# Performance work log

Hardware: AMD Instinct MI355X
Metric: run time of the kernel (lower is better)

The kernel has to match this reference:

```python
import jax, jax.numpy as jnp
import numpy as np

N, E, OBS, H, MSG, A = 20000, 640000, 64, 256, 128, 16


def setup_inputs() -> dict:
    key = jax.random.key(0)
    ks = jax.random.split(key, 16)
    s = lambda fan_in: 1.0 / np.sqrt(fan_in)
    inp = {
        'feat': jax.random.normal(ks[0], (N, OBS), jnp.float32),
        'h': jax.random.normal(ks[1], (N, H), jnp.float32),
        'src': jax.random.randint(ks[2], (E,), 0, N, jnp.int32),
        'dst': jax.random.randint(ks[3], (E,), 0, N, jnp.int32),
        # DenseObservationEncoder: 2 Linear+ReLU layers
        'enc_W0': jax.random.uniform(ks[4], (OBS, H), jnp.float32, -s(OBS), s(OBS)),
        'enc_b0': jnp.zeros((H,), jnp.float32),
        'enc_W1': jax.random.uniform(ks[5], (H, H), jnp.float32, -s(H), s(H)),
        'enc_b1': jnp.zeros((H,), jnp.float32),
        # BaseComm.f_msg: Linear(2H -> MSG)
        'msg_W': jax.random.uniform(ks[6], (2 * H, MSG), jnp.float32, -s(2 * H), s(2 * H)),
        'msg_b': jnp.zeros((MSG,), jnp.float32),
        # BaseComm.f_udt: GRUCell(H+MSG -> H), torch gate order r,z,n
        'gru_Wih': jax.random.uniform(ks[7], (H + MSG, 3 * H), jnp.float32, -s(H), s(H)),
        'gru_Whh': jax.random.uniform(ks[8], (H, 3 * H), jnp.float32, -s(H), s(H)),
        'gru_bih': jnp.zeros((3 * H,), jnp.float32),
        'gru_bhh': jnp.zeros((3 * H,), jnp.float32),
        # f_out: Linear(H -> n_actions)
        'out_W': jax.random.uniform(ks[9], (H, A), jnp.float32, -s(H), s(H)),
        'out_b': jnp.zeros((A,), jnp.float32),
    }
    return inp


def _gru_cell(u, h, Wih, Whh, bih, bhh):
    gi = u @ Wih + bih          # [N, 3H]
    gh = h @ Whh + bhh          # [N, 3H]
    i_r, i_z, i_n = jnp.split(gi, 3, axis=1)
    h_r, h_z, h_n = jnp.split(gh, 3, axis=1)
    r = jax.nn.sigmoid(i_r + h_r)
    z = jax.nn.sigmoid(i_z + h_z)
    n = jnp.tanh(i_n + r * h_n)
    return (1.0 - z) * n + z * h


def reference(feat, h, src, dst, enc_W0, enc_b0, enc_W1, enc_b1,
              msg_W, msg_b, gru_Wih, gru_Whh, gru_bih, gru_bhh,
              out_W, out_b):
    n_nodes = feat.shape[0]
    # encoder MLP
    x = jax.nn.relu(feat @ enc_W0 + enc_b0)
    x = jax.nn.relu(x @ enc_W1 + enc_b1)            # [N, H]
    h_det = jax.lax.stop_gradient(h)
    # edge messages: f_msg(cat(x[src], h_det[src])) done as split matmul to avoid the concat copy
    Wx, Wh = msg_W[:x.shape[1]], msg_W[x.shape[1]:]
    msg = x[src] @ Wx + h_det[src] @ Wh + msg_b     # [E, MSG]
    # mean aggregation into destination mailboxes (zero for isolated nodes, like DGL)
    sums = jax.ops.segment_sum(msg, dst, num_segments=n_nodes)          # [N, MSG]
    cnt = jax.ops.segment_sum(jnp.ones_like(dst, jnp.float32), dst, num_segments=n_nodes)
    c = sums / jnp.maximum(cnt, 1.0)[:, None]
    # GRU update
    u = jnp.concatenate([x, c], axis=1)             # [N, H+MSG]
    h_new = _gru_cell(u, h, gru_Wih, gru_Whh, gru_bih, gru_bhh)
    q = h_new @ out_W + out_b                       # [N, n_actions]
    return q, h_new
```

## Files before the change

### kernel.cpp

```cpp
#include <hip/hip_runtime.h>

#define N_NODES 20000
#define N_EDGES 640000
#define OBS 64
#define HDIM 256
#define MSGD 128
#define ADIM 16
#define Q_OFF 0
#define HN_OFF (N_NODES * ADIM)
#define DEG_PAD 128
#define CNT_STRIDE 16

typedef __bf16 bf16x8 __attribute__((ext_vector_type(8)));
typedef float  f32x4  __attribute__((ext_vector_type(4)));

__device__ __forceinline__ unsigned short f2bf(float f) {
    union { float f; unsigned int i; } v; v.f = f;
    unsigned int i = v.i;
    return (unsigned short)((i + 0x7fffu + ((i >> 16) & 1u)) >> 16);
}
__device__ __forceinline__ float bf2f(unsigned short u) {
    union { unsigned int i; float f; } v; v.i = ((unsigned int)u) << 16; return v.f;
}
__device__ __forceinline__ bf16x8 ld8(const unsigned short* p) {
    bf16x8 r;
    __builtin_memcpy(&r, __builtin_assume_aligned(p, 16), 16);
    return r;
}
__device__ __forceinline__ f32x4 mfma16(bf16x8 a, bf16x8 b, f32x4 c) {
    return __builtin_amdgcn_mfma_f32_16x16x32_bf16(a, b, c, 0, 0, 0);
}
__device__ __forceinline__ float sigmoidf_(float x) { return 1.0f / (1.0f + __expf(-x)); }
__device__ __forceinline__ float tanhf_(float x) { return 2.0f / (1.0f + __expf(-2.0f * x)) - 1.0f; }

__device__ __forceinline__ int packIdx(int row, int k, int Kc) {
    return ((row >> 4) * Kc + (k >> 5)) * 512 + (((k >> 3) & 3) * 16 + (row & 15)) * 8 + (k & 7);
}
__device__ __forceinline__ int packIdxEp(int tile, int rlow, int t, int lr, int Kc) {
    return (tile * Kc + (t >> 1)) * 512 + (((t & 1) * 2 + (lr >> 3)) * 16 + rlow) * 8 + (lr & 7);
}
__device__ __forceinline__ int packIdxLoc(int rlow, int t, int lr) {
    return (t >> 1) * 512 + (((t & 1) * 2 + (lr >> 3)) * 16 + rlow) * 8 + (lr & 7);
}

#define WS_W0P    0u
#define WS_W1P    32768u
#define WS_WMP    163840u
#define WS_WGP    294912u
#define WS_WOP    1277952u
#define WS_FEATP  1286144u
#define WS_HBP    3846144u
#define WS_XP     24326144u
#define WS_MN     34566144u
#define WS_CP     39686144u
#define WS_HNP    44806144u
#define WS_CNT    55046144u

#define GATE_STRIDE 163840

__global__ __launch_bounds__(256) void setup_kernel(
    const float* __restrict__ feat, const float* __restrict__ h,
    const float* __restrict__ w0, const float* __restrict__ w1, const float* __restrict__ wm,
    const float* __restrict__ wih, const float* __restrict__ whh, const float* __restrict__ wo,
    unsigned short* __restrict__ featp, unsigned short* __restrict__ hbp,
    unsigned short* __restrict__ w0p, unsigned short* __restrict__ w1p,
    unsigned short* __restrict__ wmp, unsigned short* __restrict__ wgp,
    unsigned short* __restrict__ wop)
{
    const int tid = blockIdx.x * 256 + threadIdx.x;
    const int np = gridDim.x * 256;

    for (int it = tid; it < 5000 * 8; it += np) {
        int rowq = it >> 3, kb = it & 7;
        int row0 = rowq * 4, k = kb * 8;
        uint4 vv[4];
        #pragma unroll
        for (int j = 0; j < 4; ++j) {
            const float4* p = (const float4*)(feat + (row0 + j) * OBS + k);
            float4 a = p[0], b = p[1];
            union { unsigned short u[8]; uint4 v; } r;
            r.u[0]=f2bf(a.x); r.u[1]=f2bf(a.y); r.u[2]=f2bf(a.z); r.u[3]=f2bf(a.w);
            r.u[4]=f2bf(b.x); r.u[5]=f2bf(b.y); r.u[6]=f2bf(b.z); r.u[7]=f2bf(b.w);
            vv[j] = r.v;
        }
        uint4* dp = (uint4*)(featp + packIdx(row0, k, 2));
        dp[0]=vv[0]; dp[1]=vv[1]; dp[2]=vv[2]; dp[3]=vv[3];
    }
    for (int it = tid; it < 5000 * 32; it += np) {
        int rowq = it >> 5, kb = it & 31;
        int row0 = rowq * 4, k = kb * 8;
        uint4 vv[4];
        #pragma unroll
        for (int j = 0; j < 4; ++j) {
            const float4* p = (const float4*)(h + (row0 + j) * HDIM + k);
            float4 a = p[0], b = p[1];
            union { unsigned short u[8]; uint4 v; } r;
            r.u[0]=f2bf(a.x); r.u[1]=f2bf(a.y); r.u[2]=f2bf(a.z); r.u[3]=f2bf(a.w);
            r.u[4]=f2bf(b.x); r.u[5]=f2bf(b.y); r.u[6]=f2bf(b.z); r.u[7]=f2bf(b.w);
            vv[j] = r.v;
        }
        uint4* dp = (uint4*)(hbp + packIdx(row0, k, 8));
        dp[0]=vv[0]; dp[1]=vv[1]; dp[2]=vv[2]; dp[3]=vv[3];
    }
    for (int it = tid; it < 512; it += np) {
        int nq = it & 63, kb = it >> 6;
        unsigned short u[4][8];
        #pragma unroll
        for (int j = 0; j < 8; ++j) {
            float4 f = *(const float4*)(w0 + (kb * 8 + j) * 256 + nq * 4);
            u[0][j]=f2bf(f.x); u[1][j]=f2bf(f.y); u[2][j]=f2bf(f.z); u[3][j]=f2bf(f.w);
        }
        uint4* dp = (uint4*)(w0p + packIdx(nq * 4, kb * 8, 2));
        #pragma unroll
        for (int n = 0; n < 4; ++n) { uint4 v; __builtin_memcpy(&v, u[n], 16); dp[n] = v; }
    }
    for (int it = tid; it < 2048; it += np) {
        int nq = it & 63, kb = it >> 6;
        unsigned short u[4][8];
        #pragma unroll
        for (int j = 0; j < 8; ++j) {
            float4 f = *(const float4*)(w1 + (kb * 8 + j) * 256 + nq * 4);
            u[0][j]=f2bf(f.x); u[1][j]=f2bf(f.y); u[2][j]=f2bf(f.z); u[3][j]=f2bf(f.w);
        }
        uint4* dp = (uint4*)(w1p + packIdx(nq * 4, kb * 8, 8));
        #pragma unroll
        for (int n = 0; n < 4; ++n) { uint4 v; __builtin_memcpy(&v, u[n], 16); dp[n] = v; }
    }
    for (int it = tid; it < 2048; it += np) {
        int nq = it & 31, kb = it >> 5;
        unsigned short u[4][8];
        #pragma unroll
        for (int j = 0; j < 8; ++j) {
            float4 f = *(const float4*)(wm + (kb * 8 + j) * 128 + nq * 4);
            u[0][j]=f2bf(f.x); u[1][j]=f2bf(f.y); u[2][j]=f2bf(f.z); u[3][j]=f2bf(f.w);
        }
        uint4* dp = (uint4*)(wmp + packIdx(nq * 4, kb * 8, 16));
        #pragma unroll
        for (int n = 0; n < 4; ++n) { uint4 v; __builtin_memcpy(&v, u[n], 16); dp[n] = v; }
    }
    for (int it = tid; it < 9216; it += np) {
        int c3q = it % 192, kb = it / 192;
        int n4 = c3q * 4, gate = n4 >> 8, nn = n4 & 255;
        unsigned short u[4][8];
        #pragma unroll
        for (int j = 0; j < 8; ++j) {
            float4 f = *(const float4*)(wih + (kb * 8 + j) * 768 + n4);
            u[0][j]=f2bf(f.x); u[1][j]=f2bf(f.y); u[2][j]=f2bf(f.z); u[3][j]=f2bf(f.w);
        }
        uint4* dp = (uint4*)(wgp + gate * GATE_STRIDE + packIdx(nn, kb * 8, 20));
        #pragma unroll
        for (int n = 0; n < 4; ++n) { uint4 v; __builtin_memcpy(&v, u[n], 16); dp[n] = v; }
    }
    for (int it = tid; it < 6144; it += np) {
        int c3q = it % 192, kb = it / 192;
        int n4 = c3q * 4, gate = n4 >> 8, nn = n4 & 255;
        unsigned short u[4][8];
        #pragma unroll
        for (int j = 0; j < 8; ++j) {
            float4 f = *(const float4*)(whh + (kb * 8 + j) * 768 + n4);
            u[0][j]=f2bf(f.x); u[1][j]=f2bf(f.y); u[2][j]=f2bf(f.z); u[3][j]=f2bf(f.w);
        }
        uint4* dp = (uint4*)(wgp + gate * GATE_STRIDE + packIdx(nn, 384 + kb * 8, 20));
        #pragma unroll
        for (int n = 0; n < 4; ++n) { uint4 v; __builtin_memcpy(&v, u[n], 16); dp[n] = v; }
    }
    for (int it = tid; it < 128; it += np) {
        int nq = it & 3, kb = it >> 2;
        unsigned short u[4][8];
        #pragma unroll
        for (int j = 0; j < 8; ++j) {
            float4 f = *(const float4*)(wo + (kb * 8 + j) * 16 + nq * 4);
            u[0][j]=f2bf(f.x); u[1][j]=f2bf(f.y); u[2][j]=f2bf(f.z); u[3][j]=f2bf(f.w);
        }
        uint4* dp = (uint4*)(wop + packIdx(nq * 4, kb * 8, 8));
        #pragma unroll
        for (int n = 0; n < 4; ++n) { uint4 v; __builtin_memcpy(&v, u[n], 16); dp[n] = v; }
    }
}

__global__ __launch_bounds__(256) void enc_scatter_kernel(
    const unsigned short* __restrict__ featp, const unsigned short* __restrict__ hbp,
    const unsigned short* __restrict__ w0p, const float* __restrict__ b0,
    const unsigned short* __restrict__ w1p, const float* __restrict__ b1,
    const unsigned short* __restrict__ wmp, const float* __restrict__ mb,
    unsigned short* __restrict__ Xp, unsigned short* __restrict__ Mn,
    const int* __restrict__ src, const int* __restrict__ dst,
    int* __restrict__ cnt, int* __restrict__ bucket2)
{
    __shared__ __align__(16) unsigned short x0l[2][8][512];
    __shared__ __align__(16) unsigned short x1l[2][8][512];

    if (blockIdx.x >= 626) {
        int i = (blockIdx.x - 626) * 256 + threadIdx.x;
        if (i < N_EDGES) {
            int d = dst[i];
            int rank = atomicAdd(&cnt[d * CNT_STRIDE], 1);
            if (rank < DEG_PAD) bucket2[d * DEG_PAD + rank] = src[i];
        }
        return;
    }

    const int wave = threadIdx.x >> 6;
    const int lane = threadIdx.x & 63, lr = lane & 15, lq = lane >> 4;
    const int m32 = blockIdx.x;
    int tG[2]; bool val[2];
    #pragma unroll
    for (int mf = 0; mf < 2; ++mf) { int tl = m32 * 2 + mf; val[mf] = tl < 1250; tG[mf] = val[mf] ? tl : 1249; }

    for (int i = 0; i < 4; ++i) {
        const int t = wave * 4 + i;
        f32x4 acc[2] = {{0,0,0,0},{0,0,0,0}};
        for (int c = 0; c < 2; ++c) {
            bf16x8 b = ld8(w0p + (t * 2 + c) * 512 + lane * 8);
            #pragma unroll
            for (int mf = 0; mf < 2; ++mf) {
                bf16x8 a = ld8(featp + (tG[mf] * 2 + c) * 512 + lane * 8);
                acc[mf] = mfma16(a, b, acc[mf]);
            }
        }
        float bias = b0[t * 16 + lr];
        #pragma unroll
        for (int mf = 0; mf < 2; ++mf)
            #pragma unroll
            for (int r = 0; r < 4; ++r)
                (&x0l[mf][0][0])[packIdxLoc(lq * 4 + r, t, lr)] = f2bf(fmaxf(acc[mf][r] + bias, 0.f));
    }
    __syncthreads();
    for (int i = 0; i < 4; ++i) {
        const int t = wave * 4 + i;
        f32x4 acc[2] = {{0,0,0,0},{0,0,0,0}};
        for (int c = 0; c < 8; ++c) {
            bf16x8 b = ld8(w1p + (t * 8 + c) * 512 + lane * 8);
            #pragma unroll
            for (int mf = 0; mf < 2; ++mf) {
                bf16x8 a = ld8(&x0l[mf][c][lane * 8]);
                acc[mf] = mfma16(a, b, acc[mf]);
            }
        }
        float bias = b1[t * 16 + lr];
        #pragma unroll
        for (int mf = 0; mf < 2; ++mf)
            #pragma unroll
            for (int r = 0; r < 4; ++r) {
                unsigned short xb = f2bf(fmaxf(acc[mf][r] + bias, 0.f));
                (&x1l[mf][0][0])[packIdxLoc(lq * 4 + r, t, lr)] = xb;
                if (val[mf]) Xp[packIdxEp(tG[mf], lq * 4 + r, t, lr, 8)] = xb;
            }
    }
    __syncthreads();
    for (int i = 0; i < 2; ++i) {
        const int t = wave * 2 + i;
        const int col = t * 16 + lr;
        f32x4 acc[2] = {{0,0,0,0},{0,0,0,0}};
        for (int c = 0; c < 8; ++c) {
            bf16x8 b = ld8(wmp + (t * 16 + c) * 512 + lane * 8);
            #pragma unroll
            for (int mf = 0; mf < 2; ++mf) {
                bf16x8 a = ld8(&x1l[mf][c][lane * 8]);
                acc[mf] = mfma16(a, b, acc[mf]);
            }
        }
        for (int c = 0; c < 8; ++c) {
            bf16x8 b = ld8(wmp + (t * 16 + 8 + c) * 512 + lane * 8);
            #pragma unroll
            for (int mf = 0; mf < 2; ++mf) {
                bf16x8 a = ld8(hbp + (tG[mf] * 8 + c) * 512 + lane * 8);
                acc[mf] = mfma16(a, b, acc[mf]);
            }
        }
        float bias = mb[col];
        #pragma unroll
        for (int mf = 0; mf < 2; ++mf) if (val[mf])
            #pragma unroll
            for (int r = 0; r < 4; ++r) {
                int row = m32 * 32 + mf * 16 + lq * 4 + r;
                Mn[row * MSGD + col] = f2bf(acc[mf][r] + bias);
            }
    }
}

__global__ __launch_bounds__(256) void aggregate_kernel(
    const int* __restrict__ cnt, const int* __restrict__ bucket2,
    const unsigned short* __restrict__ Mn, unsigned short* __restrict__ Cp)
{
    const int wave = threadIdx.x >> 6;
    const int lane = threadIdx.x & 63;
    const int quarter = lane >> 4;
    const int l16 = lane & 15;
    const int node = blockIdx.x * 4 + wave;
    if (node >= N_NODES) return;
    const int dg0 = cnt[node * CNT_STRIDE];
    const int dg = dg0 < DEG_PAD ? dg0 : DEG_PAD;
    const int* bk = bucket2 + node * DEG_PAD;
    float s[8] = {0.f,0.f,0.f,0.f,0.f,0.f,0.f,0.f};
    const uint4* mn4 = (const uint4*)Mn;
#define ACC8(pk) do { \
    s[0] += bf2f((unsigned short)((pk).x & 0xffffu)); s[1] += bf2f((unsigned short)((pk).x >> 16)); \
    s[2] += bf2f((unsigned short)((pk).y & 0xffffu)); s[3] += bf2f((unsigned short)((pk).y >> 16)); \
    s[4] += bf2f((unsigned short)((pk).z & 0xffffu)); s[5] += bf2f((unsigned short)((pk).z >> 16)); \
    s[6] += bf2f((unsigned short)((pk).w & 0xffffu)); s[7] += bf2f((unsigned short)((pk).w >> 16)); } while (0)
    int j = 0;
    for (; j + 8 <= dg; j += 8) {
        int ix0 = bk[j + quarter];
        int ix1 = bk[j + 4 + quarter];
        uint4 p0 = mn4[ix0 * 16 + l16];
        uint4 p1 = mn4[ix1 * 16 + l16];
        ACC8(p0); ACC8(p1);
    }
    for (; j + 4 <= dg; j += 4) {
        int ix = bk[j + quarter];
        uint4 pk = mn4[ix * 16 + l16];
        ACC8(pk);
    }
    for (; j < dg; ++j) {
        if (quarter == 0) {
            int ix = bk[j];
            uint4 pk = mn4[ix * 16 + l16];
            ACC8(pk);
        }
    }
#undef ACC8
    #pragma unroll
    for (int i = 0; i < 8; ++i) {
        s[i] += __shfl_xor(s[i], 16);
        s[i] += __shfl_xor(s[i], 32);
    }
    if (quarter == 0) {
        float invc = 1.0f / fmaxf((float)dg0, 1.0f);
        union { unsigned short u[8]; uint4 v; } r;
        #pragma unroll
        for (int i = 0; i < 8; ++i) r.u[i] = f2bf(s[i] * invc);
        *(uint4*)(Cp + packIdx(node, l16 * 8, 4)) = r.v;
    }
}

__global__ __launch_bounds__(512, 4) void gru_kernel(
    const unsigned short* __restrict__ Xp, const unsigned short* __restrict__ Cp,
    const unsigned short* __restrict__ hbp, const float* __restrict__ h,
    const unsigned short* __restrict__ wgp,
    const float* __restrict__ bih, const float* __restrict__ bhh,
    unsigned short* __restrict__ Hnp, float* __restrict__ out)
{
#define GL4(dst, ptr) asm volatile("global_load_dwordx4 %0, %1, off" : "=v"(dst) : "v"(ptr))
#define GLDW(dst, ptr, IMM) asm volatile("global_load_dword %0, %1, off offset:" #IMM : "=v"(dst) : "v"(ptr))
#define WAITV(N) do { asm volatile("s_waitcnt vmcnt(" #N ")" ::: "memory"); \
                      __builtin_amdgcn_sched_barrier(0); } while (0)
#define ISSUE2(cn) do { \
    const unsigned short *p0_, *p1_; \
    if ((cn) < 8)       { p0_ = bX + (cn) * 512;        p1_ = bX + 4096 + (cn) * 512; } \
    else if ((cn) < 12) { p0_ = bC + ((cn) - 8) * 512;  p1_ = bC + 2048 + ((cn) - 8) * 512; } \
    else                { p0_ = bH + ((cn) - 12) * 512; p1_ = bH + 4096 + ((cn) - 12) * 512; } \
    GL4(ring[(cn) & 3][0], p0_); GL4(ring[(cn) & 3][1], p1_); } while (0)
#define ISSUE1(cn) do { \
    const unsigned short *p_; \
    if ((cn) < 8)       p_ = bX + (cn) * 512; \
    else if ((cn) < 12) p_ = bC + ((cn) - 8) * 512; \
    else                p_ = bH + ((cn) - 12) * 512; \
    GL4(ring[(cn) & 3][0], p_); } while (0)
#define STEP(c, W) do { \
    bf16x8 br_ = ld8(&wlds[0][(c) * 512 + l8]); \
    bf16x8 bz_ = ld8(&wlds[1][(c) * 512 + l8]); \
    bf16x8 bn_ = ld8(&wlds[2][(c) * 512 + l8]); \
    WAITV(W); \
    bf16x8 a0_, a1_; \
    __builtin_memcpy(&a0_, &ring[(c) & 3][0], 16); \
    __builtin_memcpy(&a1_, &ring[(c) & 3][1], 16); \
    ar[0] = mfma16(a0_, br_, ar[0]);  ar[1] = mfma16(a1_, br_, ar[1]); \
    az[0] = mfma16(a0_, bz_, az[0]);  az[1] = mfma16(a1_, bz_, az[1]); \
    if ((c) < 12) { ani[0] = mfma16(a0_, bn_, ani[0]); ani[1] = mfma16(a1_, bn_, ani[1]); } \
    else          { anh[0] = mfma16(a0_, bn_, anh[0]); anh[1] = mfma16(a1_, bn_, anh[1]); } \
    if ((c) + 4 < 20) ISSUE2((c) + 4); \
    if ((c) == 15) { \
        GLDW(hov[0][0], hb0, 0); GLDW(hov[0][1], hb0, 1024); \
        GLDW(hov[0][2], hb0, 2048); GLDW(hov[0][3], hb0, 3072); \
        GLDW(hov[1][0], hb1, 0); GLDW(hov[1][1], hb1, 1024); \
        GLDW(hov[1][2], hb1, 2048); GLDW(hov[1][3], hb1, 3072); \
    } } while (0)
#define HSTEP(c, W) do { \
    bf16x8 br_ = ld8(&wlds[0][(c) * 512 + l8]); \
    bf16x8 bz_ = ld8(&wlds[1][(c) * 512 + l8]); \
    bf16x8 bn_ = ld8(&wlds[2][(c) * 512 + l8]); \
    WAITV(W); \
    bf16x8 a0_; \
    __builtin_memcpy(&a0_, &ring[(c) & 3][0], 16); \
    ar[0] = mfma16(a0_, br_, ar[0]); \
    az[0] = mfma16(a0_, bz_, az[0]); \
    if ((c) < 12) ani[0] = mfma16(a0_, bn_, ani[0]); \
    else          anh[0] = mfma16(a0_, bn_, anh[0]); \
    if ((c) + 4 < 20) ISSUE1((c) + 4); \
    if ((c) == 15) { \
        GLDW(hov[0][0], hb0, 0); GLDW(hov[0][1], hb0, 1024); \
        GLDW(hov[0][2], hb0, 2048); GLDW(hov[0][3], hb0, 3072); \
    } } while (0)
#define SETBASES32(m) do { \
    bX = Xp  + (m) * 8192 + l8; \
    bC = Cp  + (m) * 4096 + l8; \
    bH = hbp + (m) * 8192 + l8; \
    hb0 = h + ((m) * 32 + lq * 4) * HDIM + col; \
    hb1 = hb0 + 16 * HDIM; } while (0)
#define EPILOG32(m) do { \
    _Pragma("unroll") \
    for (int mf = 0; mf < 2; ++mf) \
        _Pragma("unroll") \
        for (int r = 0; r < 4; ++r) { \
            int row = (m) * 32 + mf * 16 + lq * 4 + r; \
            float rg = sigmoidf_(ar[mf][r] + bir); \
            float zg = sigmoidf_(az[mf][r] + biz); \
            float ng = tanhf_(ani[mf][r] + bin + rg * (anh[mf][r] + bhn)); \
            float hn = (1.0f - zg) * ng + zg * hov[mf][r]; \
            out[HN_OFF + row * HDIM + col] = hn; \
            Hnp[packIdxEp((m) * 2 + mf, lq * 4 + r, t, lr, 8)] = f2bf(hn); \
        } } while (0)
#define ACCINIT() do { \
    _Pragma("unroll") \
    for (int mf = 0; mf < 2; ++mf) { \
        ar[mf]  = (f32x4){0,0,0,0}; az[mf]  = (f32x4){0,0,0,0}; \
        ani[mf] = (f32x4){0,0,0,0}; anh[mf] = (f32x4){0,0,0,0}; } } while (0)

    __shared__ __align__(16) unsigned short wlds[3][10240];

    const int b = blockIdx.x;
    const int x = b & 7;
    const int i = b >> 3;
    const int t = i & 15;
    const int wi = i >> 4;
    const int tid = threadIdx.x;
    const int wv = tid >> 6;
    const int lane = tid & 63, lr = lane & 15, lq = lane >> 4;
    const int l8 = lane * 8;
    const int widx = wi * 8 + wv;
    const int start = x * 78 + (x ? 1 : 0);
    const int cnt_ = 78 + (x == 0 ? 1 : 0);
    const int col = t * 16 + lr;

    const int m32a = start + widx;
    const int m32b = start + 32 + widx;
    const int halves = 2 * (cnt_ - 64);
    const bool has_tail = widx < halves;
    const int m32t = start + 64 + (widx >> 1);
    const int hm = widx & 1;

    const unsigned short *bX, *bC, *bH;
    const float *hb0, *hb1;
    uint4 ring[4][2];
    f32x4 ar[2], az[2], ani[2], anh[2];
    float hov[2][4];

    SETBASES32(m32a);
    ISSUE2(0); ISSUE2(1); ISSUE2(2); ISSUE2(3);

    for (int s = tid; s < 3840; s += 512) {
        int g = s / 1280, rem = s - g * 1280;
        const uint4* sp = (const uint4*)(wgp + g * GATE_STRIDE + t * 10240) + rem;
        *((uint4*)(&wlds[g][0]) + rem) = *sp;
    }
    const float bir = bih[col] + bhh[col];
    const float biz = bih[256 + col] + bhh[256 + col];
    const float bin = bih[512 + col];
    const float bhn = bhh[512 + col];
    __syncthreads();

    ACCINIT();
    STEP(0, 22);  STEP(1, 22);  STEP(2, 22);  STEP(3, 22);
    STEP(4, 6);   STEP(5, 6);   STEP(6, 6);   STEP(7, 6);
    STEP(8, 6);   STEP(9, 6);   STEP(10, 6);  STEP(11, 6);
    STEP(12, 6);  STEP(13, 6);  STEP(14, 6);  STEP(15, 6);
    STEP(16, 14); STEP(17, 12); STEP(18, 10); STEP(19, 8);
    SETBASES32(m32b);
    ISSUE2(0); ISSUE2(1); ISSUE2(2); ISSUE2(3);
    WAITV(8);
    EPILOG32(m32a);

    ACCINIT();
    STEP(0, 22);  STEP(1, 22);  STEP(2, 22);  STEP(3, 22);
    STEP(4, 6);   STEP(5, 6);   STEP(6, 6);   STEP(7, 6);
    STEP(8, 6);   STEP(9, 6);   STEP(10, 6);  STEP(11, 6);
    STEP(12, 6);  STEP(13, 6);  STEP(14, 6);  STEP(15, 6);
    STEP(16, 14); STEP(17, 12); STEP(18, 10); STEP(19, 8);

    if (has_tail) {
        bX = Xp  + (m32t * 2 + hm) * 4096 + l8;
        bC = Cp  + (m32t * 2 + hm) * 2048 + l8;
        bH = hbp + (m32t * 2 + hm) * 4096 + l8;
        hb0 = h + (m32t * 32 + hm * 16 + lq * 4) * HDIM + col;
        ISSUE1(0); ISSUE1(1); ISSUE1(2); ISSUE1(3);
        WAITV(4);
        EPILOG32(m32b);
        ACCINIT();
        HSTEP(0, 19);  HSTEP(1, 19);  HSTEP(2, 19);  HSTEP(3, 19);
        HSTEP(4, 3);   HSTEP(5, 3);   HSTEP(6, 3);   HSTEP(7, 3);
        HSTEP(8, 3);   HSTEP(9, 3);   HSTEP(10, 3);  HSTEP(11, 3);
        HSTEP(12, 3);  HSTEP(13, 3);  HSTEP(14, 3);  HSTEP(15, 3);
        HSTEP(16, 7);  HSTEP(17, 6);  HSTEP(18, 5);  HSTEP(19, 4);
        WAITV(0);
        #pragma unroll
        for (int r = 0; r < 4; ++r) {
            int row = m32t * 32 + hm * 16 + lq * 4 + r;
            float rg = sigmoidf_(ar[0][r] + bir);
            float zg = sigmoidf_(az[0][r] + biz);
            float ng = tanhf_(ani[0][r] + bin + rg * (anh[0][r] + bhn));
            float hn = (1.0f - zg) * ng + zg * hov[0][r];
            out[HN_OFF + row * HDIM + col] = hn;
            Hnp[packIdxEp(m32t * 2 + hm, lq * 4 + r, t, lr, 8)] = f2bf(hn);
        }
    } else {
        WAITV(0);
        EPILOG32(m32b);
    }
#undef GL4
#undef GLDW
#undef WAITV
#undef ISSUE2
#undef ISSUE1
#undef STEP
#undef HSTEP
#undef SETBASES32
#undef EPILOG32
#undef ACCINIT
}

__global__ __launch_bounds__(256) void q_kernel(
    const unsigned short* __restrict__ Hnp, const unsigned short* __restrict__ wop,
    const float* __restrict__ ob, float* __restrict__ out)
{
    int w = blockIdx.x * 4 + (threadIdx.x >> 6);
    if (w >= 1250) w = 1249;
    const int lane = threadIdx.x & 63, lr = lane & 15, lq = lane >> 4;
    f32x4 acc = {0.f, 0.f, 0.f, 0.f};
    for (int c = 0; c < 8; ++c) {
        bf16x8 a = ld8(Hnp + (w * 8 + c) * 512 + lane * 8);
        bf16x8 b = ld8(wop + c * 512 + lane * 8);
        acc = mfma16(a, b, acc);
    }
    float bias = ob[lr];
    #pragma unroll
    for (int r = 0; r < 4; ++r)
        out[Q_OFF + (w * 16 + lq * 4 + r) * ADIM + lr] = acc[r] + bias;
}

extern "C" void kernel_launch(void* const* d_in, const int* in_sizes, int n_in,
                              void* d_out, int out_size, void* d_ws, size_t ws_size,
                              hipStream_t stream) {
    const float* feat = (const float*)d_in[0];
    const float* h    = (const float*)d_in[1];
    const int* src    = (const int*)d_in[2];
    const int* dst    = (const int*)d_in[3];
    const float* w0   = (const float*)d_in[4];
    const float* b0   = (const float*)d_in[5];
    const float* w1   = (const float*)d_in[6];
    const float* b1   = (const float*)d_in[7];
    const float* wm   = (const float*)d_in[8];
    const float* mb   = (const float*)d_in[9];
    const float* wih  = (const float*)d_in[10];
    const float* whh  = (const float*)d_in[11];
    const float* bih  = (const float*)d_in[12];
    const float* bhh  = (const float*)d_in[13];
    const float* wo   = (const float*)d_in[14];
    const float* ob   = (const float*)d_in[15];

    char* ws = (char*)d_ws;
    unsigned short* w0p   = (unsigned short*)(ws + WS_W0P);
    unsigned short* w1p   = (unsigned short*)(ws + WS_W1P);
    unsigned short* wmp   = (unsigned short*)(ws + WS_WMP);
    unsigned short* wgp   = (unsigned short*)(ws + WS_WGP);
    unsigned short* wop   = (unsigned short*)(ws + WS_WOP);
    unsigned short* featp = (unsigned short*)(ws + WS_FEATP);
    unsigned short* hbp   = (unsigned short*)(ws + WS_HBP);
    unsigned short* Xp    = (unsigned short*)(ws + WS_XP);
    unsigned short* Mn    = (unsigned short*)(ws + WS_MN);
    unsigned short* Cp    = (unsigned short*)(ws + WS_CP);
    unsigned short* Hnp   = (unsigned short*)(ws + WS_HNP);
    int* bucket2          = (int*)(ws + WS_HNP);
    int* cnt              = (int*)(ws + WS_CNT);
    float* out            = (float*)d_out;

    hipMemsetAsync(cnt, 0, N_NODES * CNT_STRIDE * sizeof(int), stream);
    hipLaunchKernelGGL(setup_kernel, dim3(2048), dim3(256), 0, stream,
                       feat, h, w0, w1, wm, wih, whh, wo,
                       featp, hbp, w0p, w1p, wmp, wgp, wop);
    hipLaunchKernelGGL(enc_scatter_kernel, dim3(626 + (N_EDGES + 255) / 256), dim3(256), 0, stream,
                       featp, hbp, w0p, b0, w1p, b1, wmp, mb, Xp, Mn,
                       src, dst, cnt, bucket2);
    hipLaunchKernelGGL(aggregate_kernel, dim3((N_NODES + 3) / 4), dim3(256), 0, stream,
                       cnt, bucket2, Mn, Cp);
    hipLaunchKernelGGL(gru_kernel, dim3(512), dim3(512), 0, stream,
                       Xp, Cp, hbp, h, wgp, bih, bhh, Hnp, out);
    hipLaunchKernelGGL(q_kernel, dim3(313), dim3(256), 0, stream, Hnp, wop, ob, out);
}
```

Measured before the change: 198.5 us.

## Fuse feat/h bf16 conversion into encoder kernel and drop packed feat buffer

Moves the fp32-to-bf16 conversion of feat and h out of the setup kernel and into the encoder/message kernel, which now loads fp32 rows directly into MFMA fragments. The packed h copy is still written for the later GRU kernel, but only as a byproduct of the message matmul. The feat staging buffer is removed and the setup kernel shrinks to an 80-block grid that only packs weights. The message loop is also restructured so each A fragment is loaded once and reused across both output tiles, trading extra register pressure for less global traffic.

```diff
diff --git a/kernel.cpp b/kernel.cpp
--- a/kernel.cpp
+++ b/kernel.cpp
@@ -27,6 +27,15 @@
     __builtin_memcpy(&r, __builtin_assume_aligned(p, 16), 16);
     return r;
 }
+__device__ __forceinline__ bf16x8 ldf8(const float* p) {
+    float4 a, b;
+    __builtin_memcpy(&a, p, 16);
+    __builtin_memcpy(&b, p + 4, 16);
+    union { unsigned short u[8]; bf16x8 v; } r;
+    r.u[0]=f2bf(a.x); r.u[1]=f2bf(a.y); r.u[2]=f2bf(a.z); r.u[3]=f2bf(a.w);
+    r.u[4]=f2bf(b.x); r.u[5]=f2bf(b.y); r.u[6]=f2bf(b.z); r.u[7]=f2bf(b.w);
+    return r.v;
+}
 __device__ __forceinline__ f32x4 mfma16(bf16x8 a, bf16x8 b, f32x4 c) {
     return __builtin_amdgcn_mfma_f32_16x16x32_bf16(a, b, c, 0, 0, 0);
 }
@@ -48,7 +57,6 @@
 #define WS_WMP    163840u
 #define WS_WGP    294912u
 #define WS_WOP    1277952u
-#define WS_FEATP  1286144u
 #define WS_HBP    3846144u
 #define WS_XP     24326144u
 #define WS_MN     34566144u
@@ -59,10 +67,8 @@
 #define GATE_STRIDE 163840
 
 __global__ __launch_bounds__(256) void setup_kernel(
-    const float* __restrict__ feat, const float* __restrict__ h,
     const float* __restrict__ w0, const float* __restrict__ w1, const float* __restrict__ wm,
     const float* __restrict__ wih, const float* __restrict__ whh, const float* __restrict__ wo,
-    unsigned short* __restrict__ featp, unsigned short* __restrict__ hbp,
     unsigned short* __restrict__ w0p, unsigned short* __restrict__ w1p,
     unsigned short* __restrict__ wmp, unsigned short* __restrict__ wgp,
     unsigned short* __restrict__ wop)
@@ -70,38 +76,6 @@
     const int tid = blockIdx.x * 256 + threadIdx.x;
     const int np = gridDim.x * 256;
 
-    for (int it = tid; it < 5000 * 8; it += np) {
-        int rowq = it >> 3, kb = it & 7;
-        int row0 = rowq * 4, k = kb * 8;
-        uint4 vv[4];
-        #pragma unroll
-        for (int j = 0; j < 4; ++j) {
-            const float4* p = (const float4*)(feat + (row0 + j) * OBS + k);
-            float4 a = p[0], b = p[1];
-            union { unsigned short u[8]; uint4 v; } r;
-            r.u[0]=f2bf(a.x); r.u[1]=f2bf(a.y); r.u[2]=f2bf(a.z); r.u[3]=f2bf(a.w);
-            r.u[4]=f2bf(b.x); r.u[5]=f2bf(b.y); r.u[6]=f2bf(b.z); r.u[7]=f2bf(b.w);
-            vv[j] = r.v;
-        }
-        uint4* dp = (uint4*)(featp + packIdx(row0, k, 2));
-        dp[0]=vv[0]; dp[1]=vv[1]; dp[2]=vv[2]; dp[3]=vv[3];
-    }
-    for (int it = tid; it < 5000 * 32; it += np) {
-        int rowq = it >> 5, kb = it & 31;
-        int row0 = rowq * 4, k = kb * 8;
-        uint4 vv[4];
-        #pragma unroll
-        for (int j = 0; j < 4; ++j) {
-            const float4* p = (const float4*)(h + (row0 + j) * HDIM + k);
-            float4 a = p[0], b = p[1];
-            union { unsigned short u[8]; uint4 v; } r;
-            r.u[0]=f2bf(a.x); r.u[1]=f2bf(a.y); r.u[2]=f2bf(a.z); r.u[3]=f2bf(a.w);
-            r.u[4]=f2bf(b.x); r.u[5]=f2bf(b.y); r.u[6]=f2bf(b.z); r.u[7]=f2bf(b.w);
-            vv[j] = r.v;
-        }
-        uint4* dp = (uint4*)(hbp + packIdx(row0, k, 8));
-        dp[0]=vv[0]; dp[1]=vv[1]; dp[2]=vv[2]; dp[3]=vv[3];
-    }
     for (int it = tid; it < 512; it += np) {
         int nq = it & 63, kb = it >> 6;
         unsigned short u[4][8];
@@ -179,10 +153,11 @@
 }
 
 __global__ __launch_bounds__(256) void enc_scatter_kernel(
-    const unsigned short* __restrict__ featp, const unsigned short* __restrict__ hbp,
+    const float* __restrict__ feat, const float* __restrict__ h,
     const unsigned short* __restrict__ w0p, const float* __restrict__ b0,
     const unsigned short* __restrict__ w1p, const float* __restrict__ b1,
     const unsigned short* __restrict__ wmp, const float* __restrict__ mb,
+    unsigned short* __restrict__ hbp,
     unsigned short* __restrict__ Xp, unsigned short* __restrict__ Mn,
     const int* __restrict__ src, const int* __restrict__ dst,
     int* __restrict__ cnt, int* __restrict__ bucket2)
@@ -202,21 +177,27 @@
 
     const int wave = threadIdx.x >> 6;
     const int lane = threadIdx.x & 63, lr = lane & 15, lq = lane >> 4;
+    const int kq = lane >> 4;
     const int m32 = blockIdx.x;
     int tG[2]; bool val[2];
     #pragma unroll
     for (int mf = 0; mf < 2; ++mf) { int tl = m32 * 2 + mf; val[mf] = tl < 1250; tG[mf] = val[mf] ? tl : 1249; }
 
+    bf16x8 aF[2][2];
+    #pragma unroll
+    for (int mf = 0; mf < 2; ++mf)
+        #pragma unroll
+        for (int c = 0; c < 2; ++c)
+            aF[mf][c] = ldf8(feat + (tG[mf] * 16 + lr) * OBS + c * 32 + kq * 8);
     for (int i = 0; i < 4; ++i) {
         const int t = wave * 4 + i;
         f32x4 acc[2] = {{0,0,0,0},{0,0,0,0}};
+        #pragma unroll
         for (int c = 0; c < 2; ++c) {
             bf16x8 b = ld8(w0p + (t * 2 + c) * 512 + lane * 8);
             #pragma unroll
-            for (int mf = 0; mf < 2; ++mf) {
-                bf16x8 a = ld8(featp + (tG[mf] * 2 + c) * 512 + lane * 8);
-                acc[mf] = mfma16(a, b, acc[mf]);
-            }
+            for (int mf = 0; mf < 2; ++mf)
+                acc[mf] = mfma16(aF[mf][c], b, acc[mf]);
         }
         float bias = b0[t * 16 + lr];
         #pragma unroll
@@ -248,33 +229,55 @@
             }
     }
     __syncthreads();
+    f32x4 acc[2][2];
+    #pragma unroll
+    for (int i = 0; i < 2; ++i)
+        #pragma unroll
+        for (int mf = 0; mf < 2; ++mf)
+            acc[i][mf] = (f32x4){0,0,0,0};
+    for (int c = 0; c < 8; ++c) {
+        bf16x8 aX[2];
+        #pragma unroll
+        for (int mf = 0; mf < 2; ++mf) aX[mf] = ld8(&x1l[mf][c][lane * 8]);
+        #pragma unroll
+        for (int i = 0; i < 2; ++i) {
+            const int t = wave * 2 + i;
+            bf16x8 b = ld8(wmp + (t * 16 + c) * 512 + lane * 8);
+            #pragma unroll
+            for (int mf = 0; mf < 2; ++mf)
+                acc[i][mf] = mfma16(aX[mf], b, acc[i][mf]);
+        }
+    }
+    for (int c = 0; c < 8; ++c) {
+        bf16x8 aH[2];
+        #pragma unroll
+        for (int mf = 0; mf < 2; ++mf) {
+            aH[mf] = ldf8(h + (tG[mf] * 16 + lr) * HDIM + c * 32 + kq * 8);
+            if (val[mf]) {
+                uint4 v; __builtin_memcpy(&v, &aH[mf], 16);
+                *(uint4*)(hbp + (tG[mf] * 8 + c) * 512 + lane * 8) = v;
+            }
+        }
+        #pragma unroll
+        for (int i = 0; i < 2; ++i) {
+            const int t = wave * 2 + i;
+            bf16x8 b = ld8(wmp + (t * 16 + 8 + c) * 512 + lane * 8);
+            #pragma unroll
+            for (int mf = 0; mf < 2; ++mf)
+                acc[i][mf] = mfma16(aH[mf], b, acc[i][mf]);
+        }
+    }
+    #pragma unroll
     for (int i = 0; i < 2; ++i) {
         const int t = wave * 2 + i;
         const int col = t * 16 + lr;
-        f32x4 acc[2] = {{0,0,0,0},{0,0,0,0}};
-        for (int c = 0; c < 8; ++c) {
-            bf16x8 b = ld8(wmp + (t * 16 + c) * 512 + lane * 8);
-            #pragma unroll
-            for (int mf = 0; mf < 2; ++mf) {
-                bf16x8 a = ld8(&x1l[mf][c][lane * 8]);
-                acc[mf] = mfma16(a, b, acc[mf]);
-            }
-        }
-        for (int c = 0; c < 8; ++c) {
-            bf16x8 b = ld8(wmp + (t * 16 + 8 + c) * 512 + lane * 8);
-            #pragma unroll
-            for (int mf = 0; mf < 2; ++mf) {
-                bf16x8 a = ld8(hbp + (tG[mf] * 8 + c) * 512 + lane * 8);
-                acc[mf] = mfma16(a, b, acc[mf]);
-            }
-        }
         float bias = mb[col];
         #pragma unroll
         for (int mf = 0; mf < 2; ++mf) if (val[mf])
             #pragma unroll
             for (int r = 0; r < 4; ++r) {
                 int row = m32 * 32 + mf * 16 + lq * 4 + r;
-                Mn[row * MSGD + col] = f2bf(acc[mf][r] + bias);
+                Mn[row * MSGD + col] = f2bf(acc[i][mf][r] + bias);
             }
     }
 }
@@ -564,7 +567,6 @@
     unsigned short* wmp   = (unsigned short*)(ws + WS_WMP);
     unsigned short* wgp   = (unsigned short*)(ws + WS_WGP);
     unsigned short* wop   = (unsigned short*)(ws + WS_WOP);
-    unsigned short* featp = (unsigned short*)(ws + WS_FEATP);
     unsigned short* hbp   = (unsigned short*)(ws + WS_HBP);
     unsigned short* Xp    = (unsigned short*)(ws + WS_XP);
     unsigned short* Mn    = (unsigned short*)(ws + WS_MN);
@@ -575,11 +577,11 @@
     float* out            = (float*)d_out;
 
     hipMemsetAsync(cnt, 0, N_NODES * CNT_STRIDE * sizeof(int), stream);
-    hipLaunchKernelGGL(setup_kernel, dim3(2048), dim3(256), 0, stream,
-                       feat, h, w0, w1, wm, wih, whh, wo,
-                       featp, hbp, w0p, w1p, wmp, wgp, wop);
+    hipLaunchKernelGGL(setup_kernel, dim3(80), dim3(256), 0, stream,
+                       w0, w1, wm, wih, whh, wo,
+                       w0p, w1p, wmp, wgp, wop);
     hipLaunchKernelGGL(enc_scatter_kernel, dim3(626 + (N_EDGES + 255) / 256), dim3(256), 0, stream,
-                       featp, hbp, w0p, b0, w1p, b1, wmp, mb, Xp, Mn,
+                       feat, h, w0p, b0, w1p, b1, wmp, mb, hbp, Xp, Mn,
                        src, dst, cnt, bucket2);
     hipLaunchKernelGGL(aggregate_kernel, dim3((N_NODES + 3) / 4), dim3(256), 0, stream,
                        cnt, bucket2, Mn, Cp);
```

Result: slower. 205.1 us (+3.3%).
